# Kernel optimization log

Measured on AMD Instinct MI355X. Metric: run time of the kernel, lower is better.

## Reference

```python
import jax, jax.numpy as jnp
import numpy as np

B, S, DIM = 2, 2048, 2048
H, KVH, HD = 16, 8, 128
NREP = H // KVH


def _make_freqs(seqlen, head_dim):
    # Rotation-matrix form of RoPE: freqs[s,0,p] = [[cos,-sin],[sin,cos]]
    pos = jnp.arange(seqlen, dtype=jnp.float32)
    inv = 1.0 / (10000.0 ** (jnp.arange(0, head_dim, 2, dtype=jnp.float32) / head_dim))
    ang = pos[:, None] * inv[None, :]                      # (S, HD/2)
    cos, sin = jnp.cos(ang), jnp.sin(ang)
    f = jnp.stack([jnp.stack([cos, -sin], -1),
                   jnp.stack([sin, cos], -1)], -2)          # (S, HD/2, 2, 2)
    return f[:, None]                                       # (S, 1, HD/2, 2, 2)


def setup_inputs() -> dict:
    key = jax.random.key(0)
    k0, k1, k2, k3, k4 = jax.random.split(key, 5)
    x = jax.random.normal(k0, (B, S, DIM), jnp.float32)
    x_mask = jnp.ones((B, S), jnp.bool_)                    # unused by forward
    freqs_cis = _make_freqs(S, HD)
    w_qkv = jax.random.normal(k1, ((H + 2 * KVH) * HD, DIM), jnp.float32) * (DIM ** -0.5)
    w_out = jax.random.normal(k2, (DIM, H * HD), jnp.float32) * ((H * HD) ** -0.5)
    q_norm_w = 1.0 + 0.02 * jax.random.normal(k3, (HD,), jnp.float32)
    k_norm_w = 1.0 + 0.02 * jax.random.normal(k4, (HD,), jnp.float32)
    return {"x": x, "x_mask": x_mask, "freqs_cis": freqs_cis,
            "w_qkv": w_qkv, "w_out": w_out,
            "q_norm_w": q_norm_w, "k_norm_w": k_norm_w}


def _rmsnorm(x, w):
    eps = jnp.asarray(jnp.finfo(x.dtype).eps, x.dtype)
    return x * jax.lax.rsqrt(jnp.mean(x * x, -1, keepdims=True) + eps) * w


def _rope(x, freqs):
    # x: (B,S,h,HD), freqs: (S,1,HD/2,2,2)
    t = x.reshape(*x.shape[:-1], HD // 2, 1, 2)
    out = freqs[..., 0] * t[..., 0] + freqs[..., 1] * t[..., 1]
    return out.reshape(x.shape)


def reference(x, x_mask, freqs_cis, w_qkv, w_out, q_norm_w, k_norm_w):
    b, s, _ = x.shape
    qkv = jnp.einsum('bsd,od->bso', x, w_qkv)
    xq, xk, xv = jnp.split(qkv, [H * HD, (H + KVH) * HD], axis=-1)
    xq = _rope(_rmsnorm(xq.reshape(b, s, H, HD), q_norm_w), freqs_cis)
    xk = _rope(_rmsnorm(xk.reshape(b, s, KVH, HD), k_norm_w), freqs_cis)
    xv = xv.reshape(b, s, KVH, HD)
    # GQA: repeat kv heads (consecutive copies, matching unsqueeze+repeat+flatten)
    xk = jnp.repeat(xk, NREP, axis=2)
    xv = jnp.repeat(xv, NREP, axis=2)
    scale = HD ** -0.5
    scores = jnp.einsum('bqhd,bkhd->bhqk', xq, xk) * scale
    attn = jax.nn.softmax(scores, axis=-1)
    out = jnp.einsum('bhqk,bkhd->bqhd', attn, xv).reshape(b, s, H * HD)
    return jnp.einsum('bso,do->bsd', out, w_out)
```

## Files before the change

### kernel.cpp

```cpp
#include <hip/hip_runtime.h>
#include <hip/hip_bf16.h>
#include <cstdint>

typedef __bf16 bf16_t;
typedef __attribute__((ext_vector_type(8)))  __bf16 bf16x8;
typedef __attribute__((ext_vector_type(4)))  float  f32x4;
typedef __attribute__((ext_vector_type(16))) float  f32x16;

#define AS1 __attribute__((address_space(1)))
#define AS3 __attribute__((address_space(3)))
#define DEV __device__ __forceinline__

DEV uint32_t pk2bf(float lo, float hi) {
  union { __bf16 h[2]; uint32_t u; } x;
  x.h[0] = (__bf16)lo; x.h[1] = (__bf16)hi; return x.u;
}

__global__ __launch_bounds__(256) void k_cvt(const float* __restrict__ in,
                                             bf16_t* __restrict__ out, int n) {
  int i = (blockIdx.x * 256 + threadIdx.x) * 4;
  if (i + 3 < n) {
    const float4 v = *reinterpret_cast<const float4*>(in + i);
    union { bf16_t h[4]; uint2 u; } o;
    o.h[0] = (bf16_t)v.x; o.h[1] = (bf16_t)v.y;
    o.h[2] = (bf16_t)v.z; o.h[3] = (bf16_t)v.w;
    *reinterpret_cast<uint2*>(out + i) = o.u;
  }
}

__global__ __launch_bounds__(256, 2) void k_gemm(
    const bf16_t* __restrict__ A, const bf16_t* __restrict__ B,
    void* __restrict__ Cv, int M, int N, int K, int out_bf16)
{
  __shared__ bf16_t Asl[2][128 * 32];
  __shared__ bf16_t Bsl[2][128 * 32];
  const int tid = threadIdx.x;
  const int w = tid >> 6, l = tid & 63;
  const int wr = w >> 1, wc = w & 1;
  const int c16 = l & 15, g = l >> 4;
  const int m0 = blockIdx.y * 128, n0 = blockIdx.x * 128;
  const bf16_t* Ab = A + (size_t)m0 * K;
  const bf16_t* Bb = B + (size_t)n0 * K;

  f32x4 acc[4][4] = {};

  auto stage = [&](int buf, int kt) {
    const bf16_t* Ag = Ab + kt * 32;
    const bf16_t* Bg = Bb + kt * 32;
#pragma unroll
    for (int i = 0; i < 2; ++i) {
      int ch = tid + 256 * i;
      int row = ch >> 2, kc = ch & 3;
      __builtin_amdgcn_global_load_lds(
          (const AS1 void*)(Ag + (size_t)row * K + kc * 8),
          (AS3 void*)(&Asl[buf][(w * 64 + 256 * i) * 8]), 16, 0, 0);
      __builtin_amdgcn_global_load_lds(
          (const AS1 void*)(Bg + (size_t)row * K + kc * 8),
          (AS3 void*)(&Bsl[buf][(w * 64 + 256 * i) * 8]), 16, 0, 0);
    }
  };

  auto compute = [&](int buf) {
    bf16x8 af[4], bfg[4];
#pragma unroll
    for (int mi = 0; mi < 4; ++mi)
      af[mi] = *reinterpret_cast<const bf16x8*>(
          &Asl[buf][(wr * 64 + mi * 16 + c16) * 32 + g * 8]);
#pragma unroll
    for (int ni = 0; ni < 4; ++ni)
      bfg[ni] = *reinterpret_cast<const bf16x8*>(
          &Bsl[buf][(wc * 64 + ni * 16 + c16) * 32 + g * 8]);
#pragma unroll
    for (int mi = 0; mi < 4; ++mi)
#pragma unroll
      for (int ni = 0; ni < 4; ++ni)
        acc[mi][ni] = __builtin_amdgcn_mfma_f32_16x16x32_bf16(
            af[mi], bfg[ni], acc[mi][ni], 0, 0, 0);
  };

  const int NT = K >> 5;
  stage(0, 0);
  __syncthreads();
  for (int kt = 0; kt < NT - 1; ++kt) {
    stage((kt + 1) & 1, kt + 1);
    compute(kt & 1);
    __syncthreads();
  }
  compute((NT - 1) & 1);

  const int row0 = m0 + wr * 64, col0 = n0 + wc * 64;
#pragma unroll
  for (int mi = 0; mi < 4; ++mi)
#pragma unroll
    for (int ni = 0; ni < 4; ++ni) {
      const int cc = col0 + ni * 16 + c16;
#pragma unroll
      for (int r = 0; r < 4; ++r) {
        const int rr = row0 + mi * 16 + g * 4 + r;
        if (out_bf16)
          ((bf16_t*)Cv)[(size_t)rr * N + cc] = (bf16_t)acc[mi][ni][r];
        else
          ((float*)Cv)[(size_t)rr * N + cc] = acc[mi][ni][r];
      }
    }
}

__global__ __launch_bounds__(256) void k_prep_qk(
    const bf16_t* __restrict__ qkv, const float* __restrict__ freqs,
    const float* __restrict__ qw, const float* __restrict__ kw,
    bf16_t* __restrict__ Qd, bf16_t* __restrict__ Kd)
{
  const int w = threadIdx.x >> 6, l = threadIdx.x & 63;
  const int R = blockIdx.x * 4 + w;
  const int j = R >> 12;
  const int token = R & 4095;
  const int s = token & 2047, b = token >> 11;
  const bool isq = (j < 16);
  const int col0 = isq ? (j << 7) : (2048 + ((j - 16) << 7));

  union { uint32_t u; __bf16 h[2]; } xin;
  xin.u = *reinterpret_cast<const uint32_t*>(qkv + (size_t)token * 4096 + col0 + 2 * l);
  float x0 = (float)xin.h[0], x1 = (float)xin.h[1];
  float ss = x0 * x0 + x1 * x1;
#pragma unroll
  for (int d = 1; d < 64; d <<= 1) ss += __shfl_xor(ss, d, 64);
  const float rn = rsqrtf(ss * (1.0f / 128.0f) + 1.1920929e-7f);
  const float2 wv = *reinterpret_cast<const float2*>((isq ? qw : kw) + 2 * l);
  const float y0 = x0 * rn * wv.x, y1 = x1 * rn * wv.y;
  const float4 f = *reinterpret_cast<const float4*>(freqs + (size_t)s * 256 + l * 4);
  float o0 = f.x * y0 + f.y * y1;
  float o1 = f.z * y0 + f.w * y1;
  if (isq) { o0 *= 0.08838834764831845f; o1 *= 0.08838834764831845f; }
  const uint32_t pk = pk2bf(o0, o1);
  if (isq)
    *reinterpret_cast<uint32_t*>(Qd + ((size_t)(b * 16 + j) * 2048 + s) * 128 + 2 * l) = pk;
  else
    *reinterpret_cast<uint32_t*>(Kd + ((size_t)(b * 8 + (j - 16)) * 2048 + s) * 128 + 2 * l) = pk;
}

__global__ __launch_bounds__(256) void k_prep_v(const bf16_t* __restrict__ qkv,
                                                bf16_t* __restrict__ Vt)
{
  __shared__ bf16_t vt[64][136];
  const int tid = threadIdx.x;
  const int bid = blockIdx.x;
  const int st = bid & 31, kh = (bid >> 5) & 7, b = bid >> 8;
  const int s0 = st * 64;
#pragma unroll
  for (int i = 0; i < 4; ++i) {
    int ch = tid + 256 * i;
    int srow = ch >> 4, d8 = ch & 15;
    bf16x8 v = *reinterpret_cast<const bf16x8*>(
        qkv + (size_t)(b * 2048 + s0 + srow) * 4096 + 3072 + kh * 128 + d8 * 8);
    *reinterpret_cast<bf16x8*>(&vt[srow][d8 * 8]) = v;
  }
  __syncthreads();
  const int d = tid >> 1, sc = tid & 1;
  bf16_t* dst = Vt + ((size_t)(b * 8 + kh) * 128 + d) * 2048 + s0 + 32 * sc;
#pragma unroll
  for (int grp = 0; grp < 4; ++grp) {
    uint32_t pk[4];
#pragma unroll
    for (int q = 0; q < 4; ++q) {
      int jj = 32 * sc + grp * 8 + q * 2;
      union { __bf16 h[2]; uint32_t u; } e;
      e.h[0] = vt[jj][d]; e.h[1] = vt[jj + 1][d];
      pk[q] = e.u;
    }
    uint4 o; o.x = pk[0]; o.y = pk[1]; o.z = pk[2]; o.w = pk[3];
    *reinterpret_cast<uint4*>(dst + grp * 8) = o;
  }
}

__global__ __launch_bounds__(256, 2) void k_attn(
    const bf16_t* __restrict__ Qd, const bf16_t* __restrict__ Kd,
    const bf16_t* __restrict__ Vt, bf16_t* __restrict__ O)
{
  __shared__ bf16_t kbuf[2][64 * 128];
  __shared__ bf16_t vbuf[2][128 * 64];
  const int tid = threadIdx.x;
  const int w = tid >> 6, l = tid & 63;
  const int c = l & 31, h2 = l >> 5;
  const int bid = blockIdx.x;
  const int qt = bid & 15, h = (bid >> 4) & 15, b = bid >> 8;
  const int kvh = h >> 1;
  const bf16_t* Qg = Qd + ((size_t)(b * 16 + h) * 2048 + qt * 128 + w * 32) * 128;
  const bf16_t* Kg = Kd + ((size_t)(b * 8 + kvh) * 2048) * 128;
  const bf16_t* Vg = Vt + ((size_t)(b * 8 + kvh) * 128) * 2048;

  bf16x8 qf[8];
#pragma unroll
  for (int s = 0; s < 8; ++s)
    qf[s] = *reinterpret_cast<const bf16x8*>(Qg + (size_t)c * 128 + s * 16 + h2 * 8);

  f32x16 oacc[4] = {};
  float mrun = -3.0e38f, lrun = 0.0f;

  auto stage = [&](int buf, int kt) {
#pragma unroll
    for (int i = 0; i < 4; ++i) {
      int ch = tid + 256 * i;
      {
        int key = ch >> 4, d16 = ch & 15;
        int soff = key * 256 + ((d16 * 16) ^ ((key & 7) << 4));
        __builtin_amdgcn_global_load_lds(
            (const AS1 void*)((const char*)Kg + (size_t)kt * 64 * 256 + soff),
            (AS3 void*)((char*)&kbuf[buf][0] + (w * 64 + 256 * i) * 16), 16, 0, 0);
      }
      {
        int d = ch >> 3, k8 = (ch & 7) ^ (d & 7);
        __builtin_amdgcn_global_load_lds(
            (const AS1 void*)(Vg + (size_t)d * 2048 + kt * 64 + k8 * 8),
            (AS3 void*)((char*)&vbuf[buf][0] + (w * 64 + 256 * i) * 16), 16, 0, 0);
      }
    }
  };

  auto compute = [&](int buf) {
    f32x16 sacc[2] = {};
    const char* kb = (const char*)&kbuf[buf][0];
    __builtin_amdgcn_s_setprio(1);
#pragma unroll
    for (int m = 0; m < 2; ++m)
#pragma unroll
      for (int s = 0; s < 8; ++s) {
        int byte = (m * 32 + c) * 256 + ((s * 32 + h2 * 16) ^ ((c & 7) << 4));
        bf16x8 kf = *reinterpret_cast<const bf16x8*>(kb + byte);
        sacc[m] = __builtin_amdgcn_mfma_f32_32x32x16_bf16(kf, qf[s], sacc[m], 0, 0, 0);
      }
    __builtin_amdgcn_s_setprio(0);

    float pmax = -3.0e38f;
#pragma unroll
    for (int m = 0; m < 2; ++m)
#pragma unroll
      for (int r = 0; r < 16; ++r) pmax = fmaxf(pmax, sacc[m][r]);
    pmax = fmaxf(pmax, __shfl_xor(pmax, 32, 64));
    if (!__all(pmax - mrun <= 8.0f)) {
      const float mnew = fmaxf(mrun, pmax);
      const float corr = __expf(mrun - mnew);
      lrun *= corr;
#pragma unroll
      for (int df = 0; df < 4; ++df)
#pragma unroll
        for (int r = 0; r < 16; ++r) oacc[df][r] *= corr;
      mrun = mnew;
    }
    float psum = 0.0f;
#pragma unroll
    for (int m = 0; m < 2; ++m)
#pragma unroll
      for (int r = 0; r < 16; ++r) {
        float p = __expf(sacc[m][r] - mrun);
        sacc[m][r] = p;
        psum += p;
      }
    psum += __shfl_xor(psum, 32, 64);
    lrun += psum;

    const char* vb = (const char*)&vbuf[buf][0];
#pragma unroll
    for (int t = 0; t < 4; ++t) {
      const int m = t >> 1, q2 = t & 1;
      uint32_t u0 = pk2bf(sacc[m][8 * q2 + 0], sacc[m][8 * q2 + 1]);
      uint32_t u1 = pk2bf(sacc[m][8 * q2 + 2], sacc[m][8 * q2 + 3]);
      uint32_t u2 = pk2bf(sacc[m][8 * q2 + 4], sacc[m][8 * q2 + 5]);
      uint32_t u3 = pk2bf(sacc[m][8 * q2 + 6], sacc[m][8 * q2 + 7]);
      auto r02 = __builtin_amdgcn_permlane32_swap((int)u0, (int)u2, false, false);
      auto r13 = __builtin_amdgcn_permlane32_swap((int)u1, (int)u3, false, false);
      union { uint32_t u[4]; bf16x8 v; } pb;
      pb.u[0] = (uint32_t)r02[0]; pb.u[1] = (uint32_t)r13[0];
      pb.u[2] = (uint32_t)r02[1]; pb.u[3] = (uint32_t)r13[1];
      __builtin_amdgcn_s_setprio(1);
#pragma unroll
      for (int df = 0; df < 4; ++df) {
        int byte = (df * 32 + c) * 128 + ((t * 32 + h2 * 16) ^ ((c & 7) << 4));
        bf16x8 vf = *reinterpret_cast<const bf16x8*>(vb + byte);
        oacc[df] = __builtin_amdgcn_mfma_f32_32x32x16_bf16(vf, pb.v, oacc[df], 0, 0, 0);
      }
      __builtin_amdgcn_s_setprio(0);
    }
  };

  stage(0, 0);
  __syncthreads();
  for (int kt = 0; kt < 31; ++kt) {
    stage((kt + 1) & 1, kt + 1);
    compute(kt & 1);
    __syncthreads();
  }
  compute(1);

  const float inv = 1.0f / lrun;
  bf16_t* Og = O + ((size_t)(b * 2048 + qt * 128 + w * 32 + c) * 2048) + h * 128;
#pragma unroll
  for (int df = 0; df < 4; ++df)
#pragma unroll
    for (int rg = 0; rg < 4; ++rg) {
      uint32_t w0 = pk2bf(oacc[df][rg * 4 + 0] * inv, oacc[df][rg * 4 + 1] * inv);
      uint32_t w1 = pk2bf(oacc[df][rg * 4 + 2] * inv, oacc[df][rg * 4 + 3] * inv);
      uint2 ww; ww.x = w0; ww.y = w1;
      *reinterpret_cast<uint2*>(Og + df * 32 + 8 * rg + 4 * h2) = ww;
    }
}

extern "C" void kernel_launch(void* const* d_in, const int* in_sizes, int n_in,
                              void* d_out, int out_size, void* d_ws, size_t ws_size,
                              hipStream_t stream)
{
  const float* x     = (const float*)d_in[0];
  const float* freqs = (const float*)d_in[2];
  const float* wqkv  = (const float*)d_in[3];
  const float* wout  = (const float*)d_in[4];
  const float* qw    = (const float*)d_in[5];
  const float* kw    = (const float*)d_in[6];
  float* out = (float*)d_out;

  bf16_t* Xb   = (bf16_t*)d_ws;
  bf16_t* Wqb  = Xb  + 8388608;
  bf16_t* Wob  = Wqb + 8388608;
  bf16_t* qkvb = Wob + 4194304;
  bf16_t* Qdp  = qkvb + 16777216;
  bf16_t* Kdp  = Qdp + 8388608;
  bf16_t* Vtp  = Kdp + 4194304;
  bf16_t* Ob   = qkvb;

  k_cvt<<<8192, 256, 0, stream>>>(x, Xb, 8388608);
  k_cvt<<<8192, 256, 0, stream>>>(wqkv, Wqb, 8388608);
  k_cvt<<<4096, 256, 0, stream>>>(wout, Wob, 4194304);
  k_gemm<<<dim3(32, 32), 256, 0, stream>>>(Xb, Wqb, qkvb, 4096, 4096, 2048, 1);
  k_prep_qk<<<24576, 256, 0, stream>>>(qkvb, freqs, qw, kw, Qdp, Kdp);
  k_prep_v<<<512, 256, 0, stream>>>(qkvb, Vtp);
  k_attn<<<512, 256, 0, stream>>>(Qdp, Kdp, Vtp, Ob);
  k_gemm<<<dim3(16, 32), 256, 0, stream>>>(Ob, Wob, out, 4096, 2048, 2048, 0);
}
```

Before: 263.1 us.

## Add 256x256-tile 8-wave GEMM for QKV projection with XCD-aware block remap

Adds a new 256x256-tile GEMM kernel with 512 threads, 128 KB dynamic LDS, double buffering, swizzled LDS reads, and interleaved staging and MFMA phases separated by barriers. It is used for the QKV projection. The existing 128-tile GEMM switches to a 1D grid with a remap that spreads consecutive tiles across the 8 XCDs for better L2 locality. The attention softmax max and sum reductions are split into four independent accumulators to shorten dependency chains. The larger tile is meant to raise arithmetic intensity, but it lowers occupancy and adds barrier overhead.

```diff
diff --git a/kernel.cpp b/kernel.cpp
--- a/kernel.cpp
+++ b/kernel.cpp
@@ -10,6 +10,10 @@
 #define AS1 __attribute__((address_space(1)))
 #define AS3 __attribute__((address_space(3)))
 #define DEV __device__ __forceinline__
+
+#define S_BARRIER() asm volatile("s_barrier" ::: "memory")
+#define VMCNT0()    asm volatile("s_waitcnt vmcnt(0)" ::: "memory")
+#define SCHED0()    __builtin_amdgcn_sched_barrier(0)
 
 DEV uint32_t pk2bf(float lo, float hi) {
   union { __bf16 h[2]; uint32_t u; } x;
@@ -28,6 +32,143 @@
   }
 }
 
+#define RD_A_PAIR(dst, base, MF)                                          \
+  _Pragma("unroll") for (int j_ = 0; j_ < 2; ++j_)                        \
+  _Pragma("unroll") for (int kk_ = 0; kk_ < 2; ++kk_) {                   \
+    int p_ = (wm*128 + ((MF)+j_)*16 + c16)*128 + kk_*64 + g*16;           \
+    p_ ^= ((p_>>9)&1)<<5;                                                 \
+    dst[j_][kk_] = *reinterpret_cast<const bf16x8*>((const char*)(base) + p_); }
+
+#define RD_B_ALL(dst, base)                                               \
+  _Pragma("unroll") for (int i_ = 0; i_ < 4; ++i_)                        \
+  _Pragma("unroll") for (int kk_ = 0; kk_ < 2; ++kk_) {                   \
+    int p_ = (wn*64 + i_*16 + c16)*128 + kk_*64 + g*16;                   \
+    p_ ^= ((p_>>9)&1)<<5;                                                 \
+    dst[i_][kk_] = *reinterpret_cast<const bf16x8*>((const char*)(base) + p_); }
+
+#define MM_PAIR(aa, MF)                                                   \
+  _Pragma("unroll") for (int j_ = 0; j_ < 2; ++j_)                        \
+  _Pragma("unroll") for (int i_ = 0; i_ < 4; ++i_)                        \
+  _Pragma("unroll") for (int kk_ = 0; kk_ < 2; ++kk_)                     \
+    acc[(MF)+j_][i_] = __builtin_amdgcn_mfma_f32_16x16x32_bf16(           \
+        aa[j_][kk_], bF[i_][kk_], acc[(MF)+j_][i_], 0, 0, 0);
+
+#define STAGE_A(dstbase, half, tt)                                        \
+  _Pragma("unroll") for (int j_ = 0; j_ < 2; ++j_)                        \
+    __builtin_amdgcn_global_load_lds(                                     \
+        (const AS1 void*)(Ag + srcA[half][j_] + (tt)*64),                 \
+        (AS3 void*)((char*)(dstbase) + ((half)*1024 + 512*j_ + wuni)*16), \
+        16, 0, 0);
+
+#define STAGE_B(dstbase, half, tt)                                        \
+  _Pragma("unroll") for (int j_ = 0; j_ < 2; ++j_)                        \
+    __builtin_amdgcn_global_load_lds(                                     \
+        (const AS1 void*)(Bg + srcB[half][j_] + (tt)*64),                 \
+        (AS3 void*)((char*)(dstbase) + ((half)*1024 + 512*j_ + wuni)*16), \
+        16, 0, 0);
+
+__global__ __launch_bounds__(512, 2) void k_gemm256(
+    const bf16_t* __restrict__ Ag, const bf16_t* __restrict__ Bg,
+    void* __restrict__ Cv, int M, int N, int K, int out_bf16)
+{
+  extern __shared__ char smemraw[];
+  const int tid = threadIdx.x;
+  const int w = tid >> 6, l = tid & 63;
+  const int wm = w >> 2, wn = w & 3;
+  const int c16 = l & 15, g = l >> 4;
+  const int wuni = tid & 0x1C0;
+
+  const int nwg = gridDim.x, cpx = nwg >> 3;
+  const int bid = blockIdx.x;
+  const int L = (bid & 7) * cpx + (bid >> 3);
+  const int nbx = N >> 8;
+  const int m0 = (L / nbx) * 256, n0 = (L % nbx) * 256;
+
+  int srcA[2][2], srcB[2][2];
+#pragma unroll
+  for (int half = 0; half < 2; ++half)
+#pragma unroll
+    for (int j = 0; j < 2; ++j) {
+      int ch = half * 1024 + 512 * j + tid;
+      int cc = ch ^ (((ch >> 5) & 1) << 1);
+      int row = cc >> 3, c8 = (cc & 7) * 8;
+      srcA[half][j] = (m0 + row) * K + c8;
+      srcB[half][j] = (n0 + row) * K + c8;
+    }
+
+  f32x4 acc[8][4] = {};
+  bf16x8 aA[2][2], aB[2][2], bF[4][2];
+
+  char* const Ab0 = smemraw;
+  char* const Ab1 = smemraw + 32768;
+  char* const Bb0 = smemraw + 65536;
+  char* const Bb1 = smemraw + 98304;
+
+  const int NT = K >> 6;
+
+  STAGE_A(Ab0, 0, 0); STAGE_A(Ab0, 1, 0);
+  STAGE_B(Bb0, 0, 0); STAGE_B(Bb0, 1, 0);
+  VMCNT0();
+  S_BARRIER();
+  RD_A_PAIR(aA, Ab0, 0);
+  RD_B_ALL(bF, Bb0);
+
+#pragma unroll 1
+  for (int t = 0; t < NT; ++t) {
+    char* const Asp = (t & 1) ? Ab1 : Ab0;
+    char* const Bsp = (t & 1) ? Bb1 : Bb0;
+    char* const Asn = (t & 1) ? Ab0 : Ab1;
+    char* const Bsn = (t & 1) ? Bb0 : Bb1;
+    const bool more = (t + 1 < NT);
+
+    RD_A_PAIR(aB, Asp, 2);
+    if (more) { STAGE_A(Asn, 0, t + 1); STAGE_A(Asn, 1, t + 1); }
+    S_BARRIER();
+    __builtin_amdgcn_s_setprio(1);
+    MM_PAIR(aA, 0);
+    __builtin_amdgcn_s_setprio(0); SCHED0();
+    S_BARRIER();
+
+    RD_A_PAIR(aA, Asp, 4);
+    if (more) { STAGE_B(Bsn, 0, t + 1); STAGE_B(Bsn, 1, t + 1); }
+    S_BARRIER();
+    __builtin_amdgcn_s_setprio(1);
+    MM_PAIR(aB, 2);
+    __builtin_amdgcn_s_setprio(0); SCHED0();
+    S_BARRIER();
+
+    RD_A_PAIR(aB, Asp, 6);
+    S_BARRIER();
+    __builtin_amdgcn_s_setprio(1);
+    MM_PAIR(aA, 4);
+    __builtin_amdgcn_s_setprio(0); SCHED0();
+    S_BARRIER();
+
+    if (more) { VMCNT0(); }
+    S_BARRIER();
+    __builtin_amdgcn_s_setprio(1);
+    MM_PAIR(aB, 6);
+    __builtin_amdgcn_s_setprio(0); SCHED0();
+    if (more) { RD_A_PAIR(aA, Asn, 0); RD_B_ALL(bF, Bsn); }
+    S_BARRIER();
+  }
+
+#pragma unroll
+  for (int mf = 0; mf < 8; ++mf)
+#pragma unroll
+    for (int nf = 0; nf < 4; ++nf) {
+      const int cc = n0 + wn * 64 + nf * 16 + c16;
+#pragma unroll
+      for (int r = 0; r < 4; ++r) {
+        const int rr = m0 + wm * 128 + mf * 16 + g * 4 + r;
+        if (out_bf16)
+          ((bf16_t*)Cv)[(size_t)rr * N + cc] = (bf16_t)acc[mf][nf][r];
+        else
+          ((float*)Cv)[(size_t)rr * N + cc] = acc[mf][nf][r];
+      }
+    }
+}
+
 __global__ __launch_bounds__(256, 2) void k_gemm(
     const bf16_t* __restrict__ A, const bf16_t* __restrict__ B,
     void* __restrict__ Cv, int M, int N, int K, int out_bf16)
@@ -38,7 +179,13 @@
   const int w = tid >> 6, l = tid & 63;
   const int wr = w >> 1, wc = w & 1;
   const int c16 = l & 15, g = l >> 4;
-  const int m0 = blockIdx.y * 128, n0 = blockIdx.x * 128;
+
+  const int nwg = gridDim.x, cpx = nwg >> 3;
+  const int bid = blockIdx.x;
+  const int L = (bid & 7) * cpx + (bid >> 3);
+  const int nbx = N >> 7;
+  const int m0 = (L / nbx) * 128, n0 = (L % nbx) * 128;
+
   const bf16_t* Ab = A + (size_t)m0 * K;
   const bf16_t* Bb = B + (size_t)n0 * K;
 
@@ -230,11 +377,15 @@
       }
     __builtin_amdgcn_s_setprio(0);
 
-    float pmax = -3.0e38f;
+    float q0 = -3.0e38f, q1 = -3.0e38f, q2 = -3.0e38f, q3 = -3.0e38f;
 #pragma unroll
     for (int m = 0; m < 2; ++m)
 #pragma unroll
-      for (int r = 0; r < 16; ++r) pmax = fmaxf(pmax, sacc[m][r]);
+      for (int r = 0; r < 16; r += 4) {
+        q0 = fmaxf(q0, sacc[m][r + 0]); q1 = fmaxf(q1, sacc[m][r + 1]);
+        q2 = fmaxf(q2, sacc[m][r + 2]); q3 = fmaxf(q3, sacc[m][r + 3]);
+      }
+    float pmax = fmaxf(fmaxf(q0, q1), fmaxf(q2, q3));
     pmax = fmaxf(pmax, __shfl_xor(pmax, 32, 64));
     if (!__all(pmax - mrun <= 8.0f)) {
       const float mnew = fmaxf(mrun, pmax);
@@ -246,26 +397,31 @@
         for (int r = 0; r < 16; ++r) oacc[df][r] *= corr;
       mrun = mnew;
     }
-    float psum = 0.0f;
+    float s0 = 0.f, s1 = 0.f, s2 = 0.f, s3 = 0.f;
 #pragma unroll
     for (int m = 0; m < 2; ++m)
 #pragma unroll
-      for (int r = 0; r < 16; ++r) {
-        float p = __expf(sacc[m][r] - mrun);
-        sacc[m][r] = p;
-        psum += p;
-      }
+      for (int r = 0; r < 16; r += 4) {
+        float p0 = __expf(sacc[m][r + 0] - mrun);
+        float p1 = __expf(sacc[m][r + 1] - mrun);
+        float p2 = __expf(sacc[m][r + 2] - mrun);
+        float p3 = __expf(sacc[m][r + 3] - mrun);
+        sacc[m][r + 0] = p0; sacc[m][r + 1] = p1;
+        sacc[m][r + 2] = p2; sacc[m][r + 3] = p3;
+        s0 += p0; s1 += p1; s2 += p2; s3 += p3;
+      }
+    float psum = (s0 + s1) + (s2 + s3);
     psum += __shfl_xor(psum, 32, 64);
     lrun += psum;
 
     const char* vb = (const char*)&vbuf[buf][0];
 #pragma unroll
     for (int t = 0; t < 4; ++t) {
-      const int m = t >> 1, q2 = t & 1;
-      uint32_t u0 = pk2bf(sacc[m][8 * q2 + 0], sacc[m][8 * q2 + 1]);
-      uint32_t u1 = pk2bf(sacc[m][8 * q2 + 2], sacc[m][8 * q2 + 3]);
-      uint32_t u2 = pk2bf(sacc[m][8 * q2 + 4], sacc[m][8 * q2 + 5]);
-      uint32_t u3 = pk2bf(sacc[m][8 * q2 + 6], sacc[m][8 * q2 + 7]);
+      const int m = t >> 1, q2i = t & 1;
+      uint32_t u0 = pk2bf(sacc[m][8 * q2i + 0], sacc[m][8 * q2i + 1]);
+      uint32_t u1 = pk2bf(sacc[m][8 * q2i + 2], sacc[m][8 * q2i + 3]);
+      uint32_t u2 = pk2bf(sacc[m][8 * q2i + 4], sacc[m][8 * q2i + 5]);
+      uint32_t u3 = pk2bf(sacc[m][8 * q2i + 6], sacc[m][8 * q2i + 7]);
       auto r02 = __builtin_amdgcn_permlane32_swap((int)u0, (int)u2, false, false);
       auto r13 = __builtin_amdgcn_permlane32_swap((int)u1, (int)u3, false, false);
       union { uint32_t u[4]; bf16x8 v; } pb;
@@ -325,12 +481,15 @@
   bf16_t* Vtp  = Kdp + 4194304;
   bf16_t* Ob   = qkvb;
 
+  (void)hipFuncSetAttribute((const void*)k_gemm256,
+                            hipFuncAttributeMaxDynamicSharedMemorySize, 131072);
+
   k_cvt<<<8192, 256, 0, stream>>>(x, Xb, 8388608);
   k_cvt<<<8192, 256, 0, stream>>>(wqkv, Wqb, 8388608);
   k_cvt<<<4096, 256, 0, stream>>>(wout, Wob, 4194304);
-  k_gemm<<<dim3(32, 32), 256, 0, stream>>>(Xb, Wqb, qkvb, 4096, 4096, 2048, 1);
+  k_gemm256<<<256, 512, 131072, stream>>>(Xb, Wqb, qkvb, 4096, 4096, 2048, 1);
   k_prep_qk<<<24576, 256, 0, stream>>>(qkvb, freqs, qw, kw, Qdp, Kdp);
   k_prep_v<<<512, 256, 0, stream>>>(qkvb, Vtp);
   k_attn<<<512, 256, 0, stream>>>(Qdp, Kdp, Vtp, Ob);
-  k_gemm<<<dim3(16, 32), 256, 0, stream>>>(Ob, Wob, out, 4096, 2048, 2048, 0);
-}
+  k_gemm<<<512, 256, 0, stream>>>(Ob, Wob, out, 4096, 2048, 2048, 0);
+}
```

After: 246.0 us. -6.5%, faster.
